# Kernel optimization log

Hardware: AMD Instinct MI355X
Metric: run time of the kernel (lower is better)

The kernel has to match this reference:

```python
import jax, jax.numpy as jnp
import numpy as np

# model geometry (matches init_kwargs cfg)
D = 768        # D_EMB
PATCH = 16
T = 8192
N = T // PATCH # 512 patch tokens
H = 12         # heads
HD = D // H    # 64 head dim
NL = 6         # layers
DFF = 4 * D
B = 8
LN_EPS = 1e-5


def setup_inputs() -> dict:
    key = jax.random.key(0)
    ks = iter(jax.random.split(key, 32))
    def g(shape, scale=0.02):
        return jax.random.normal(next(ks), shape, jnp.float32) * scale
    return dict(
        x=jax.random.normal(next(ks), (B, T), jnp.float32),
        pp_w=g((D, PATCH)), pp_b=jnp.zeros((D,), jnp.float32),
        pe=g((N, D)),
        ln1_g=jnp.ones((NL, D), jnp.float32), ln1_b=jnp.zeros((NL, D), jnp.float32),
        qkv_w=g((NL, 3 * D, D)), out_w=g((NL, D, D)),
        ln2_g=jnp.ones((NL, D), jnp.float32), ln2_b=jnp.zeros((NL, D), jnp.float32),
        fc1_w=g((NL, DFF, D)), fc2_w=g((NL, D, DFF)),
        lnf_g=jnp.ones((D,), jnp.float32), lnf_b=jnp.zeros((D,), jnp.float32),
        h1_w=g((D // 2, D)), h1_b=jnp.zeros((D // 2,), jnp.float32),
        h2_w=g((2, D // 2)), h2_b=jnp.zeros((2,), jnp.float32),
    )


def _ln(x, g, b):
    m = x.mean(-1, keepdims=True)
    v = ((x - m) ** 2).mean(-1, keepdims=True)
    return (x - m) / jnp.sqrt(v + LN_EPS) * g + b


def reference(x, pp_w, pp_b, pe, ln1_g, ln1_b, qkv_w, out_w,
              ln2_g, ln2_b, fc1_w, fc2_w, lnf_g, lnf_b,
              h1_w, h1_b, h2_w, h2_b):
    Bx = x.shape[0]
    # patch embed: [B, N, PATCH] @ W^T + b -> [B, N, D]
    z = jnp.einsum('bnp,dp->bnd', x[:, :N * PATCH].reshape(Bx, N, PATCH), pp_w) + pp_b
    z = z + pe  # positional embedding (arange indexes whole table)
    mask = jnp.tril(jnp.ones((N, N), dtype=bool))
    for i in range(NL):
        # --- attention (manual causal softmax, dropout=eval/no-op) ---
        h = _ln(z, ln1_g[i], ln1_b[i])
        qkv = jnp.einsum('bnd,ed->bne', h, qkv_w[i])            # [B,N,3D]
        qkv = qkv.reshape(Bx, N, 3, H, HD).transpose(2, 0, 3, 1, 4)
        q, k, v = qkv[0], qkv[1], qkv[2]                         # [B,H,N,HD]
        s = jnp.einsum('bhld,bhmd->bhlm', q, k) / np.sqrt(HD)
        s = jnp.where(mask, s, -jnp.inf)
        a = jax.nn.softmax(s, axis=-1)
        o = jnp.einsum('bhlm,bhmd->bhld', a, v)
        o = o.transpose(0, 2, 1, 3).reshape(Bx, N, D)
        z = z + jnp.einsum('bnd,ed->bne', o, out_w[i])
        # --- FFN (exact gelu, matching F.gelu default) ---
        h = _ln(z, ln2_g[i], ln2_b[i])
        f = jax.nn.gelu(jnp.einsum('bnd,fd->bnf', h, fc1_w[i]), approximate=False)
        z = z + jnp.einsum('bnf,df->bnd', f, fc2_w[i])
    enc = _ln(z, lnf_g, lnf_b).mean(axis=1)                      # [B, D]
    y = jax.nn.relu(enc @ h1_w.T + h1_b)
    return y @ h2_w.T + h2_b                                     # [B, 2]
```

## Files before the change

### kernel.cpp

```cpp
#include <hip/hip_runtime.h>
#include <hip/hip_bf16.h>
#include <math.h>

#define D_EMB 768
#define NPATCH 16
#define NTOK 512
#define NHEAD 12
#define HDIM 64
#define NLAYER 6
#define DFF 3072
#define BATCH 8
#define MTOK (BATCH * NTOK)

typedef __attribute__((ext_vector_type(8))) short bf16x8;
typedef __attribute__((ext_vector_type(4))) float f32x4;

__device__ __forceinline__ float bf2f(ushort s) {
    unsigned u = ((unsigned)s) << 16;
    return __builtin_bit_cast(float, u);
}
__device__ __forceinline__ ushort f2bf(float f) {
    unsigned u = __builtin_bit_cast(unsigned, f);
    unsigned r = (u + 0x7FFFu + ((u >> 16) & 1u)) >> 16;
    return (ushort)r;
}

__global__ __launch_bounds__(256)
void f2bf4_kernel(const float* __restrict__ s0, ushort* __restrict__ d0, int n0,
                  const float* __restrict__ s1, ushort* __restrict__ d1, int n1,
                  const float* __restrict__ s2, ushort* __restrict__ d2, int n2,
                  const float* __restrict__ s3, ushort* __restrict__ d3, int n3)
{
    int i = blockIdx.x * 256 + threadIdx.x;
    const float* s; ushort* d; int off;
    if (i < n0)                { s = s0; d = d0; off = i; }
    else if (i < n0 + n1)      { s = s1; d = d1; off = i - n0; }
    else if (i < n0 + n1 + n2) { s = s2; d = d2; off = i - n0 - n1; }
    else if (i < n0 + n1 + n2 + n3) { s = s3; d = d3; off = i - n0 - n1 - n2; }
    else return;
    float4 v = *(const float4*)(s + (size_t)off * 4);
    ushort4 o;
    o.x = f2bf(v.x); o.y = f2bf(v.y); o.z = f2bf(v.z); o.w = f2bf(v.w);
    *(ushort4*)(d + (size_t)off * 4) = o;
}

__global__ __launch_bounds__(256)
void patch_embed_kernel(const float* __restrict__ x, const float* __restrict__ pw,
                        const float* __restrict__ pb, const float* __restrict__ pe,
                        float* __restrict__ z)
{
    int bn = blockIdx.x;
    int b = bn >> 9, n = bn & 511;
    __shared__ float xs[NPATCH];
    int t = threadIdx.x;
    if (t < NPATCH) xs[t] = x[(size_t)b * 8192 + n * NPATCH + t];
    __syncthreads();
    for (int d = t; d < D_EMB; d += 256) {
        float acc = pb[d] + pe[(size_t)n * D_EMB + d];
        const float* w = pw + (size_t)d * NPATCH;
        #pragma unroll
        for (int p = 0; p < NPATCH; ++p) acc += xs[p] * w[p];
        z[(size_t)bn * D_EMB + d] = acc;
    }
}

__device__ __forceinline__ float block_reduce_sum_256(float v)
{
    __shared__ float lds[4];
    #pragma unroll
    for (int o = 32; o > 0; o >>= 1) v += __shfl_xor(v, o);
    int lane = threadIdx.x & 63, wid = threadIdx.x >> 6;
    __syncthreads();
    if (lane == 0) lds[wid] = v;
    __syncthreads();
    return lds[0] + lds[1] + lds[2] + lds[3];
}

__device__ __forceinline__ void store_val(float* p, float v)  { *p = v; }
__device__ __forceinline__ void store_val(ushort* p, float v) { *p = f2bf(v); }

template<typename OT>
__global__ __launch_bounds__(256)
void ln_kernel(const float* __restrict__ x, const float* __restrict__ g,
               const float* __restrict__ bta, OT* __restrict__ y)
{
    int row = blockIdx.x;
    const float* xr = x + (size_t)row * D_EMB;
    int t = threadIdx.x;
    float vals[3];
    float s = 0.f;
    #pragma unroll
    for (int i = 0; i < 3; ++i) { vals[i] = xr[t + i * 256]; s += vals[i]; }
    float mean = block_reduce_sum_256(s) * (1.0f / D_EMB);
    float ss = 0.f;
    #pragma unroll
    for (int i = 0; i < 3; ++i) { float d = vals[i] - mean; ss += d * d; }
    float var = block_reduce_sum_256(ss) * (1.0f / D_EMB);
    float rstd = rsqrtf(var + 1e-5f);
    #pragma unroll
    for (int i = 0; i < 3; ++i) {
        int d = t + i * 256;
        store_val(y + (size_t)row * D_EMB + d, (vals[i] - mean) * rstd * g[d] + bta[d]);
    }
}

template<int EPI, typename OT, bool SPLITK>
__global__ __launch_bounds__(256)
void mfma_gemm(const ushort* __restrict__ A,
               const ushort* __restrict__ W,
               OT* __restrict__ C,
               const float* __restrict__ res,
               int N, int K, int lda)
{
    __shared__ ushort As[128 * 64];
    __shared__ ushort Bs[128 * 64];

    int gx = gridDim.x, gy = gridDim.y;
    int bx = blockIdx.x, by = blockIdx.y;
    int bz = SPLITK ? blockIdx.z : 0;
    if ((gy & 7) == 0) {
        int flat = bx + gx * (by + gy * bz);
        int xcd = flat & 7, j = flat >> 3;
        int ry = gy >> 3;
        by = xcd * ry + (j % ry);
        int rem = j / ry;
        bx = rem % gx;
        bz = rem / gx;
    }
    int bm = by * 128, bn = bx * 128;

    const ushort* Ab = A + (size_t)bz * K;
    const ushort* Wb = W + (size_t)bz * K;
    OT* Cb = C;

    int tid = threadIdx.x;
    int w = tid >> 6, l = tid & 63;
    int wr = w >> 1, wc = w & 1;
    int lr = l & 15, lg = l >> 4;
    f32x4 acc[4][4] = {};

    int srow = w * 32 + (l >> 3);
    int pcol = l & 7;

    for (int k0 = 0; k0 < K; k0 += 64) {
        #pragma unroll
        for (int j = 0; j < 4; ++j) {
            int row = srow + j * 8;
            int lcol = pcol ^ (row & 7);
            const ushort* sa = Ab + (size_t)(bm + row) * lda + k0 + (lcol << 3);
            const ushort* sb = Wb + (size_t)(bn + row) * lda + k0 + (lcol << 3);
            __builtin_amdgcn_global_load_lds(
                (const __attribute__((address_space(1))) unsigned int*)sa,
                (__attribute__((address_space(3))) unsigned int*)&As[row * 64 + (pcol << 3)],
                16, 0, 0);
            __builtin_amdgcn_global_load_lds(
                (const __attribute__((address_space(1))) unsigned int*)sb,
                (__attribute__((address_space(3))) unsigned int*)&Bs[row * 64 + (pcol << 3)],
                16, 0, 0);
        }
        __syncthreads();

        #pragma unroll
        for (int kk = 0; kk < 64; kk += 32) {
            int c = (kk >> 3) + lg;
            bf16x8 a[4], b[4];
            #pragma unroll
            for (int m = 0; m < 4; ++m) {
                int row = wr * 64 + m * 16 + lr;
                a[m] = *(const bf16x8*)(&As[row * 64 + ((c ^ (row & 7)) << 3)]);
            }
            #pragma unroll
            for (int n = 0; n < 4; ++n) {
                int row = wc * 64 + n * 16 + lr;
                b[n] = *(const bf16x8*)(&Bs[row * 64 + ((c ^ (row & 7)) << 3)]);
            }
            #pragma unroll
            for (int m = 0; m < 4; ++m)
                #pragma unroll
                for (int n = 0; n < 4; ++n)
                    acc[m][n] = __builtin_amdgcn_mfma_f32_16x16x32_bf16(a[m], b[n], acc[m][n], 0, 0, 0);
        }
        __syncthreads();
    }

    int r0 = lg * 4;
    #pragma unroll
    for (int m = 0; m < 4; ++m) {
        #pragma unroll
        for (int n = 0; n < 4; ++n) {
            #pragma unroll
            for (int j = 0; j < 4; ++j) {
                int gm = bm + wr * 64 + m * 16 + r0 + j;
                int gn = bn + wc * 64 + n * 16 + lr;
                float v = acc[m][n][j];
                if (EPI == 1) v = 0.5f * v * (1.0f + erff(v * 0.70710678118654752f));
                if (EPI == 2) v += res[(size_t)gm * N + gn];
                if (EPI == 3) {
                    atomicAdd((float*)&Cb[(size_t)gm * N + gn], v);
                } else {
                    store_val(Cb + (size_t)gm * N + gn, v);
                }
            }
        }
    }
}

__global__ __launch_bounds__(256)
void attn_mfma_kernel(const ushort* __restrict__ qkv, ushort* __restrict__ o)
{
    int w = threadIdx.x >> 6, l = threadIdx.x & 63;
    int qt = blockIdx.x * 4 + w;
    int h = blockIdx.y, b = blockIdx.z;
    int q0 = qt * 16;
    int lr = l & 15, lg = l >> 4;

    const size_t rs = 3 * D_EMB;
    const ushort* qbase = qkv + ((size_t)(b * NTOK)) * rs + h * HDIM;
    const ushort* kbase = qbase + D_EMB;
    const ushort* vbase = qbase + 2 * D_EMB;

    bf16x8 qf[2];
    qf[0] = *(const bf16x8*)(qbase + (size_t)(q0 + lr) * rs + lg * 8);
    qf[1] = *(const bf16x8*)(qbase + (size_t)(q0 + lr) * rs + 32 + lg * 8);

    f32x4 oacc[4] = {};
    float m_j[4], l_j[4];
    #pragma unroll
    for (int j = 0; j < 4; ++j) { m_j[j] = -1e30f; l_j[j] = 0.f; }

    __shared__ ushort P_lds[4][16][40];

    int ntiles = q0 / 32 + 1;
    for (int mt = 0; mt < ntiles; ++mt) {
        int m0 = mt * 32;
        f32x4 s[2] = {};
        #pragma unroll
        for (int kb = 0; kb < 2; ++kb) {
            const ushort* kr = kbase + (size_t)(m0 + kb * 16 + lr) * rs;
            bf16x8 k0 = *(const bf16x8*)(kr + lg * 8);
            bf16x8 k1 = *(const bf16x8*)(kr + 32 + lg * 8);
            s[kb] = __builtin_amdgcn_mfma_f32_16x16x32_bf16(qf[0], k0, s[kb], 0, 0, 0);
            s[kb] = __builtin_amdgcn_mfma_f32_16x16x32_bf16(qf[1], k1, s[kb], 0, 0, 0);
        }
        bool partial = (m0 + 31 > q0);
        float p[2][4], mx[4];
        #pragma unroll
        for (int j = 0; j < 4; ++j) {
            int qr = q0 + lg * 4 + j;
            float s0 = s[0][j] * 0.125f;
            float s1 = s[1][j] * 0.125f;
            if (partial) {
                if (m0 + lr > qr)      s0 = -1e30f;
                if (m0 + 16 + lr > qr) s1 = -1e30f;
            }
            p[0][j] = s0; p[1][j] = s1;
            float mm = fmaxf(s0, s1);
            mm = fmaxf(mm, __shfl_xor(mm, 1));
            mm = fmaxf(mm, __shfl_xor(mm, 2));
            mm = fmaxf(mm, __shfl_xor(mm, 4));
            mm = fmaxf(mm, __shfl_xor(mm, 8));
            mx[j] = mm;
        }
        #pragma unroll
        for (int j = 0; j < 4; ++j) {
            float mnew = fmaxf(m_j[j], mx[j]);
            float scale = __expf(m_j[j] - mnew);
            float p0 = __expf(p[0][j] - mnew);
            float p1 = __expf(p[1][j] - mnew);
            p[0][j] = p0; p[1][j] = p1;
            float rsum = p0 + p1;
            rsum += __shfl_xor(rsum, 1);
            rsum += __shfl_xor(rsum, 2);
            rsum += __shfl_xor(rsum, 4);
            rsum += __shfl_xor(rsum, 8);
            l_j[j] = l_j[j] * scale + rsum;
            m_j[j] = mnew;
            #pragma unroll
            for (int i = 0; i < 4; ++i) oacc[i][j] *= scale;
        }
        #pragma unroll
        for (int kb = 0; kb < 2; ++kb)
            #pragma unroll
            for (int j = 0; j < 4; ++j)
                P_lds[w][lg * 4 + j][kb * 16 + lr] = f2bf(p[kb][j]);
        asm volatile("s_waitcnt lgkmcnt(0)" ::: "memory");
        bf16x8 pa = *(const bf16x8*)(&P_lds[w][lr][lg * 8]);
        #pragma unroll
        for (int i = 0; i < 4; ++i) {
            bf16x8 vf;
            const ushort* vp = vbase + (size_t)(m0 + lg * 8) * rs + i * 16 + lr;
            #pragma unroll
            for (int j = 0; j < 8; ++j) vf[j] = (short)vp[(size_t)j * rs];
            oacc[i] = __builtin_amdgcn_mfma_f32_16x16x32_bf16(pa, vf, oacc[i], 0, 0, 0);
        }
    }
    #pragma unroll
    for (int i = 0; i < 4; ++i) {
        #pragma unroll
        for (int j = 0; j < 4; ++j) {
            int qr = q0 + lg * 4 + j;
            int d  = i * 16 + lr;
            float v = oacc[i][j] / l_j[j];
            o[((size_t)(b * NTOK + qr)) * D_EMB + h * HDIM + d] = f2bf(v);
        }
    }
}

__global__ void mean_kernel(const float* __restrict__ x, float* __restrict__ enc)
{
    int b = blockIdx.x; int d = threadIdx.x;
    float s = 0.f;
    for (int n = 0; n < NTOK; ++n) s += x[((size_t)(b * NTOK + n)) * D_EMB + d];
    enc[b * D_EMB + d] = s * (1.0f / NTOK);
}

__global__ void head1_kernel(const float* __restrict__ enc, const float* __restrict__ w,
                             const float* __restrict__ bias, float* __restrict__ r)
{
    int b = blockIdx.x; int j = threadIdx.x;
    float acc = bias[j];
    const float* e = enc + b * D_EMB;
    const float* wr = w + (size_t)j * D_EMB;
    for (int k = 0; k < D_EMB; ++k) acc += e[k] * wr[k];
    r[b * 384 + j] = fmaxf(acc, 0.f);
}

__global__ void head2_kernel(const float* __restrict__ r, const float* __restrict__ w,
                             const float* __restrict__ bias, float* __restrict__ out)
{
    int idx = threadIdx.x;
    if (idx >= 16) return;
    int b = idx >> 1, j = idx & 1;
    float acc = bias[j];
    for (int k = 0; k < 384; ++k) acc += r[b * 384 + k] * w[j * 384 + k];
    out[b * 2 + j] = acc;
}

extern "C" void kernel_launch(void* const* d_in, const int* in_sizes, int n_in,
                              void* d_out, int out_size, void* d_ws, size_t ws_size,
                              hipStream_t stream)
{
    const float* x     = (const float*)d_in[0];
    const float* pp_w  = (const float*)d_in[1];
    const float* pp_b  = (const float*)d_in[2];
    const float* pe    = (const float*)d_in[3];
    const float* ln1_g = (const float*)d_in[4];
    const float* ln1_b = (const float*)d_in[5];
    const float* qkv_w = (const float*)d_in[6];
    const float* out_w = (const float*)d_in[7];
    const float* ln2_g = (const float*)d_in[8];
    const float* ln2_b = (const float*)d_in[9];
    const float* fc1_w = (const float*)d_in[10];
    const float* fc2_w = (const float*)d_in[11];
    const float* lnf_g = (const float*)d_in[12];
    const float* lnf_b = (const float*)d_in[13];
    const float* h1_w  = (const float*)d_in[14];
    const float* h1_b  = (const float*)d_in[15];
    const float* h2_w  = (const float*)d_in[16];
    const float* h2_b  = (const float*)d_in[17];
    float* out = (float*)d_out;

    char* p = (char*)d_ws;
    float*  z      = (float*)p;  p += (size_t)MTOK * D_EMB * 4;
    ushort* big_bf = (ushort*)p; p += (size_t)MTOK * DFF * 2;
    ushort* h_bf   = (ushort*)p; p += (size_t)MTOK * D_EMB * 2;
    ushort* wq_bf  = (ushort*)p; p += (size_t)3 * D_EMB * D_EMB * 2;
    ushort* wo_bf  = (ushort*)p; p += (size_t)D_EMB * D_EMB * 2;
    ushort* wf1_bf = (ushort*)p; p += (size_t)DFF * D_EMB * 2;
    ushort* wf2_bf = (ushort*)p; p += (size_t)D_EMB * DFF * 2;
    float*  enc    = (float*)p;  p += BATCH * D_EMB * 4;
    float*  r1     = (float*)p;  p += BATCH * 384 * 4;
    float*  lnf_out = (float*)big_bf;

    patch_embed_kernel<<<MTOK, 256, 0, stream>>>(x, pp_w, pp_b, pe, z);

    const int nq = 3 * D_EMB * D_EMB, no = D_EMB * D_EMB, nf = DFF * D_EMB;
    const int n4q = nq / 4, n4o = no / 4, n4f = nf / 4;
    const int cvt_blocks = (n4q + n4o + 2 * n4f + 255) / 256;

    for (int i = 0; i < NLAYER; ++i) {
        f2bf4_kernel<<<cvt_blocks, 256, 0, stream>>>(
            qkv_w + (size_t)i * nq, wq_bf,  n4q,
            out_w + (size_t)i * no, wo_bf,  n4o,
            fc1_w + (size_t)i * nf, wf1_bf, n4f,
            fc2_w + (size_t)i * nf, wf2_bf, n4f);

        ln_kernel<ushort><<<MTOK, 256, 0, stream>>>(z, ln1_g + i * D_EMB, ln1_b + i * D_EMB, h_bf);

        dim3 gq((3 * D_EMB) / 128, MTOK / 128);
        mfma_gemm<0, ushort, false><<<gq, 256, 0, stream>>>(h_bf, wq_bf, big_bf, nullptr,
                                                            3 * D_EMB, D_EMB, D_EMB);

        dim3 ga(NTOK / 64, NHEAD, BATCH);
        attn_mfma_kernel<<<ga, 256, 0, stream>>>(big_bf, h_bf);

        dim3 gp(D_EMB / 128, MTOK / 128, 2);
        mfma_gemm<3, float, true><<<gp, 256, 0, stream>>>(h_bf, wo_bf, z, nullptr,
                                                          D_EMB, D_EMB / 2, D_EMB);

        ln_kernel<ushort><<<MTOK, 256, 0, stream>>>(z, ln2_g + i * D_EMB, ln2_b + i * D_EMB, h_bf);

        dim3 g1(DFF / 128, MTOK / 128);
        mfma_gemm<1, ushort, false><<<g1, 256, 0, stream>>>(h_bf, wf1_bf, big_bf, nullptr,
                                                            DFF, D_EMB, D_EMB);

        dim3 g2(D_EMB / 128, MTOK / 128, 2);
        mfma_gemm<3, float, true><<<g2, 256, 0, stream>>>(big_bf, wf2_bf, z, nullptr,
                                                          D_EMB, DFF / 2, DFF);
    }

    ln_kernel<float><<<MTOK, 256, 0, stream>>>(z, lnf_g, lnf_b, lnf_out);
    mean_kernel<<<BATCH, D_EMB, 0, stream>>>(lnf_out, enc);
    head1_kernel<<<BATCH, 384, 0, stream>>>(enc, h1_w, h1_b, r1);
    head2_kernel<<<1, 64, 0, stream>>>(r1, h2_w, h2_b, out);
}
```

Measured before the change: 1.225 ms.

## Switch GEMMs to 256x256 double-buffered tiles with 512 threads and split-K 4

Replaces the 128x128 single-buffered GEMM with a 256x256 tile kernel using 8 waves, double-buffered LDS staging so the next K-slice loads while the current one computes, and raised MFMA priority through setprio. The residual GEMMs move from split-K 2 to split-K 4 to keep block counts up. The aim is more data reuse per tile and overlap of memory with compute. The cost is far fewer blocks per launch (144-192 against roughly 256 CUs), more atomic traffic, and one block per CU.

```diff
diff --git a/kernel.cpp b/kernel.cpp
--- a/kernel.cpp
+++ b/kernel.cpp
@@ -104,16 +104,61 @@
     }
 }
 
+#define STAGE256(buf, k0)                                                          \
+    {                                                                              \
+        _Pragma("unroll")                                                          \
+        for (int j = 0; j < 4; ++j) {                                              \
+            int row = j * 64 + srow;                                               \
+            int lcol = pcol ^ (row & 7);                                           \
+            const ushort* sa = Ab + (size_t)(bm + row) * lda + (k0) + (lcol << 3); \
+            const ushort* sb = Wb + (size_t)(bn + row) * lda + (k0) + (lcol << 3); \
+            __builtin_amdgcn_global_load_lds(                                      \
+                (const __attribute__((address_space(1))) unsigned int*)sa,         \
+                (__attribute__((address_space(3))) unsigned int*)&As[buf][row * 64 + (pcol << 3)], \
+                16, 0, 0);                                                         \
+            __builtin_amdgcn_global_load_lds(                                      \
+                (const __attribute__((address_space(1))) unsigned int*)sb,         \
+                (__attribute__((address_space(3))) unsigned int*)&Bs[buf][row * 64 + (pcol << 3)], \
+                16, 0, 0);                                                         \
+        }                                                                          \
+    }
+
+#define COMPUTE256(buf)                                                            \
+    {                                                                              \
+        _Pragma("unroll")                                                          \
+        for (int kk = 0; kk < 2; ++kk) {                                           \
+            int c = kk * 4 + lg;                                                   \
+            bf16x8 a[8], b[4];                                                     \
+            _Pragma("unroll")                                                      \
+            for (int m = 0; m < 8; ++m) {                                          \
+                int row = wr * 128 + m * 16 + lr;                                  \
+                a[m] = *(const bf16x8*)(&As[buf][row * 64 + ((c ^ (row & 7)) << 3)]); \
+            }                                                                      \
+            _Pragma("unroll")                                                      \
+            for (int n = 0; n < 4; ++n) {                                          \
+                int row = wc * 64 + n * 16 + lr;                                   \
+                b[n] = *(const bf16x8*)(&Bs[buf][row * 64 + ((c ^ (row & 7)) << 3)]); \
+            }                                                                      \
+            __builtin_amdgcn_s_setprio(1);                                         \
+            _Pragma("unroll")                                                      \
+            for (int m = 0; m < 8; ++m) {                                          \
+                _Pragma("unroll")                                                  \
+                for (int n = 0; n < 4; ++n)                                        \
+                    acc[m][n] = __builtin_amdgcn_mfma_f32_16x16x32_bf16(a[m], b[n], acc[m][n], 0, 0, 0); \
+            }                                                                      \
+            __builtin_amdgcn_s_setprio(0);                                         \
+        }                                                                          \
+    }
+
 template<int EPI, typename OT, bool SPLITK>
-__global__ __launch_bounds__(256)
-void mfma_gemm(const ushort* __restrict__ A,
-               const ushort* __restrict__ W,
-               OT* __restrict__ C,
-               const float* __restrict__ res,
-               int N, int K, int lda)
-{
-    __shared__ ushort As[128 * 64];
-    __shared__ ushort Bs[128 * 64];
+__global__ __launch_bounds__(512, 1)
+void mfma_gemm256(const ushort* __restrict__ A,
+                  const ushort* __restrict__ W,
+                  OT* __restrict__ C,
+                  int N, int K, int lda)
+{
+    __shared__ ushort As[2][256 * 64];
+    __shared__ ushort Bs[2][256 * 64];
 
     int gx = gridDim.x, gy = gridDim.y;
     int bx = blockIdx.x, by = blockIdx.y;
@@ -127,78 +172,46 @@
         bx = rem % gx;
         bz = rem / gx;
     }
-    int bm = by * 128, bn = bx * 128;
+    int bm = by * 256, bn = bx * 256;
 
     const ushort* Ab = A + (size_t)bz * K;
     const ushort* Wb = W + (size_t)bz * K;
-    OT* Cb = C;
 
     int tid = threadIdx.x;
     int w = tid >> 6, l = tid & 63;
-    int wr = w >> 1, wc = w & 1;
+    int wr = w >> 2, wc = w & 3;
     int lr = l & 15, lg = l >> 4;
-    f32x4 acc[4][4] = {};
-
-    int srow = w * 32 + (l >> 3);
+    f32x4 acc[8][4] = {};
+
+    int srow = w * 8 + (l >> 3);
     int pcol = l & 7;
 
-    for (int k0 = 0; k0 < K; k0 += 64) {
-        #pragma unroll
-        for (int j = 0; j < 4; ++j) {
-            int row = srow + j * 8;
-            int lcol = pcol ^ (row & 7);
-            const ushort* sa = Ab + (size_t)(bm + row) * lda + k0 + (lcol << 3);
-            const ushort* sb = Wb + (size_t)(bn + row) * lda + k0 + (lcol << 3);
-            __builtin_amdgcn_global_load_lds(
-                (const __attribute__((address_space(1))) unsigned int*)sa,
-                (__attribute__((address_space(3))) unsigned int*)&As[row * 64 + (pcol << 3)],
-                16, 0, 0);
-            __builtin_amdgcn_global_load_lds(
-                (const __attribute__((address_space(1))) unsigned int*)sb,
-                (__attribute__((address_space(3))) unsigned int*)&Bs[row * 64 + (pcol << 3)],
-                16, 0, 0);
-        }
+    const int nk = K >> 6;
+    STAGE256(0, 0);
+    __syncthreads();
+    int cur = 0;
+    for (int t = 0; t < nk - 1; ++t) {
+        STAGE256(cur ^ 1, (t + 1) << 6);
+        COMPUTE256(cur);
         __syncthreads();
-
-        #pragma unroll
-        for (int kk = 0; kk < 64; kk += 32) {
-            int c = (kk >> 3) + lg;
-            bf16x8 a[4], b[4];
-            #pragma unroll
-            for (int m = 0; m < 4; ++m) {
-                int row = wr * 64 + m * 16 + lr;
-                a[m] = *(const bf16x8*)(&As[row * 64 + ((c ^ (row & 7)) << 3)]);
-            }
-            #pragma unroll
-            for (int n = 0; n < 4; ++n) {
-                int row = wc * 64 + n * 16 + lr;
-                b[n] = *(const bf16x8*)(&Bs[row * 64 + ((c ^ (row & 7)) << 3)]);
-            }
-            #pragma unroll
-            for (int m = 0; m < 4; ++m)
-                #pragma unroll
-                for (int n = 0; n < 4; ++n)
-                    acc[m][n] = __builtin_amdgcn_mfma_f32_16x16x32_bf16(a[m], b[n], acc[m][n], 0, 0, 0);
-        }
-        __syncthreads();
-    }
-
-    int r0 = lg * 4;
-    #pragma unroll
-    for (int m = 0; m < 4; ++m) {
+        cur ^= 1;
+    }
+    COMPUTE256(cur);
+
+    #pragma unroll
+    for (int m = 0; m < 8; ++m) {
         #pragma unroll
         for (int n = 0; n < 4; ++n) {
             #pragma unroll
             for (int j = 0; j < 4; ++j) {
-                int gm = bm + wr * 64 + m * 16 + r0 + j;
+                int gm = bm + wr * 128 + m * 16 + lg * 4 + j;
                 int gn = bn + wc * 64 + n * 16 + lr;
                 float v = acc[m][n][j];
                 if (EPI == 1) v = 0.5f * v * (1.0f + erff(v * 0.70710678118654752f));
-                if (EPI == 2) v += res[(size_t)gm * N + gn];
                 if (EPI == 3) {
-                    atomicAdd((float*)&Cb[(size_t)gm * N + gn], v);
+                    atomicAdd((float*)&C[(size_t)gm * N + gn], v);
                 } else {
-                    store_val(Cb + (size_t)gm * N + gn, v);
+                    store_val(C + (size_t)gm * N + gn, v);
                 }
             }
         }
@@ -387,26 +400,26 @@
 
         ln_kernel<ushort><<<MTOK, 256, 0, stream>>>(z, ln1_g + i * D_EMB, ln1_b + i * D_EMB, h_bf);
 
-        dim3 gq((3 * D_EMB) / 128, MTOK / 128);
-        mfma_gemm<0, ushort, false><<<gq, 256, 0, stream>>>(h_bf, wq_bf, big_bf, nullptr,
-                                                            3 * D_EMB, D_EMB, D_EMB);
+        dim3 gq((3 * D_EMB) / 256, MTOK / 256);
+        mfma_gemm256<0, ushort, false><<<gq, 512, 0, stream>>>(h_bf, wq_bf, big_bf,
+                                                               3 * D_EMB, D_EMB, D_EMB);
 
         dim3 ga(NTOK / 64, NHEAD, BATCH);
         attn_mfma_kernel<<<ga, 256, 0, stream>>>(big_bf, h_bf);
 
-        dim3 gp(D_EMB / 128, MTOK / 128, 2);
-        mfma_gemm<3, float, true><<<gp, 256, 0, stream>>>(h_bf, wo_bf, z, nullptr,
-                                                          D_EMB, D_EMB / 2, D_EMB);
+        dim3 gp(D_EMB / 256, MTOK / 256, 4);
+        mfma_gemm256<3, float, true><<<gp, 512, 0, stream>>>(h_bf, wo_bf, z,
+                                                             D_EMB, D_EMB / 4, D_EMB);
 
         ln_kernel<ushort><<<MTOK, 256, 0, stream>>>(z, ln2_g + i * D_EMB, ln2_b + i * D_EMB, h_bf);
 
-        dim3 g1(DFF / 128, MTOK / 128);
-        mfma_gemm<1, ushort, false><<<g1, 256, 0, stream>>>(h_bf, wf1_bf, big_bf, nullptr,
-                                                            DFF, D_EMB, D_EMB);
-
-        dim3 g2(D_EMB / 128, MTOK / 128, 2);
-        mfma_gemm<3, float, true><<<g2, 256, 0, stream>>>(big_bf, wf2_bf, z, nullptr,
-                                                          D_EMB, DFF / 2, DFF);
+        dim3 g1(DFF / 256, MTOK / 256);
+        mfma_gemm256<1, ushort, false><<<g1, 512, 0, stream>>>(h_bf, wf1_bf, big_bf,
+                                                               DFF, D_EMB, D_EMB);
+
+        dim3 g2(D_EMB / 256, MTOK / 256, 4);
+        mfma_gemm256<3, float, true><<<g2, 512, 0, stream>>>(big_bf, wf2_bf, z,
+                                                             D_EMB, DFF / 4, DFF);
     }
 
     ln_kernel<float><<<MTOK, 256, 0, stream>>>(z, lnf_g, lnf_b, lnf_out);
```

Measured after the change: 1.640 ms. 33.8% more time.
